# Performance work log

Hardware: AMD Instinct MI355X
Metric: run time of the kernel (lower is better)

The kernel has to match this reference:

```python
import jax, jax.numpy as jnp
import numpy as np

NC = 64
B, H, W = 32, 128, 128


def setup_inputs() -> dict:
    key = jax.random.key(0)
    kx, = jax.random.split(key, 1)
    x = jax.random.normal(kx, (B, NC, H, W), dtype=jnp.float32)
    # params as initialized in the torch module
    exp_param = jnp.eye(NC, dtype=jnp.float32)[:, :, None, None]  # (nc, nc, 1, 1)
    bias = jnp.zeros((NC, 1, 1), dtype=jnp.float32)               # (nc, 1, 1)
    return {"x": x, "exp_param": exp_param, "bias": bias}


def reference(x, exp_param, bias):
    # x: (B, nc, H, W); exp_param: (nc, nc, 1, 1); bias: (nc, 1, 1)
    xr = jax.nn.relu(x) + 0.1  # strictly positive -> log is safe
    # prod_i xr[b,i,h,w] ** E[i,j]  ==  exp( sum_i E[i,j] * log xr[b,i,h,w] )
    # Fused form avoids materializing the (B, nc, nc, H, W) intermediate.
    E = exp_param[:, :, 0, 0]  # (nc_in=i, nc_out=j)
    logx = jnp.log(xr)
    out = jnp.exp(jnp.einsum('bihw,ij->bjhw', logx, E)) + bias  # (B, nc, H, W)
    return out
```

## Files before the change

### kernel.cpp

```cpp
#include <hip/hip_runtime.h>

#define NCH 64
#define JT 32
#define NPASS (NCH / JT)
#define HWSZ 16384
#define NPOINTS (32 * HWSZ)

__global__ __launch_bounds__(256, 4) void fused_log_einsum_exp(
    const float* __restrict__ x,
    const float* __restrict__ E,
    const float* __restrict__ bias,
    float* __restrict__ out)
{
    const int p  = blockIdx.x * 256 + threadIdx.x;
    const int b  = p >> 14;
    const int hw = p & (HWSZ - 1);

    const float* xp = x   + (size_t)b * NCH * HWSZ + hw;
    float*       op = out + (size_t)b * NCH * HWSZ + hw;

    #pragma unroll 1
    for (int jt = 0; jt < NPASS; ++jt) {
        const float* Ej = E + jt * JT;

        float acc[JT];
        #pragma unroll
        for (int j = 0; j < JT; ++j) acc[j] = 0.0f;

        #pragma unroll 4
        for (int i = 0; i < NCH; ++i) {
            float v  = xp[(size_t)i * HWSZ];
            float lx = __logf(fmaxf(v, 0.0f) + 0.1f);
            #pragma unroll
            for (int j = 0; j < JT; ++j)
                acc[j] = fmaf(lx, Ej[i * NCH + j], acc[j]);
        }

        #pragma unroll
        for (int j = 0; j < JT; ++j)
            op[(size_t)(jt * JT + j) * HWSZ] = __expf(acc[j]) + bias[jt * JT + j];
    }
}

extern "C" void kernel_launch(void* const* d_in, const int* in_sizes, int n_in,
                              void* d_out, int out_size, void* d_ws, size_t ws_size,
                              hipStream_t stream) {
    const float* x    = (const float*)d_in[0];
    const float* E    = (const float*)d_in[1];
    const float* bias = (const float*)d_in[2];
    float* out = (float*)d_out;

    dim3 grid(NPOINTS / 256), block(256);
    hipLaunchKernelGGL(fused_log_einsum_exp, grid, block, 0, stream,
                       x, E, bias, out);
}
```

Before: 268.4 us.

## Cache all log values in registers and compute outputs row-wise via transposed E

Each thread now loads all 64 input channels once and keeps their logs in registers, instead of rereading x and recomputing the log in each of two output passes. The output loop now runs over j, so a small pre-kernel transposes E into workspace and each output row reads a contiguous E row. The dot product uses four partial accumulators. This halves global reads of x and the log work, but adds a second launch and raises register pressure against launch_bounds(256,4).

```diff
diff --git a/kernel.cpp b/kernel.cpp
--- a/kernel.cpp
+++ b/kernel.cpp
@@ -1,14 +1,24 @@
 #include <hip/hip_runtime.h>
 
 #define NCH 64
-#define JT 32
-#define NPASS (NCH / JT)
 #define HWSZ 16384
 #define NPOINTS (32 * HWSZ)
 
+__global__ __launch_bounds__(256) void transpose_E_kernel(
+    const float* __restrict__ E, float* __restrict__ ET)
+{
+    const int t = threadIdx.x;
+    #pragma unroll
+    for (int k = 0; k < 16; ++k) {
+        const int o = k * 256 + t;
+        const int j = o >> 6, i = o & 63;
+        ET[o] = E[i * NCH + j];
+    }
+}
+
 __global__ __launch_bounds__(256, 4) void fused_log_einsum_exp(
     const float* __restrict__ x,
-    const float* __restrict__ E,
+    const float* __restrict__ ET,
     const float* __restrict__ bias,
     float* __restrict__ out)
 {
@@ -19,26 +29,24 @@
     const float* xp = x   + (size_t)b * NCH * HWSZ + hw;
     float*       op = out + (size_t)b * NCH * HWSZ + hw;
 
+    float lx[NCH];
+    #pragma unroll
+    for (int i = 0; i < NCH; ++i) lx[i] = xp[(size_t)i * HWSZ];
+    #pragma unroll
+    for (int i = 0; i < NCH; ++i) lx[i] = __logf(fmaxf(lx[i], 0.0f) + 0.1f);
+
     #pragma unroll 1
-    for (int jt = 0; jt < NPASS; ++jt) {
-        const float* Ej = E + jt * JT;
-
-        float acc[JT];
+    for (int j = 0; j < NCH; ++j) {
+        const float* Er = ET + j * NCH;
+        float a0 = 0.f, a1 = 0.f, a2 = 0.f, a3 = 0.f;
         #pragma unroll
-        for (int j = 0; j < JT; ++j) acc[j] = 0.0f;
-
-        #pragma unroll 4
-        for (int i = 0; i < NCH; ++i) {
-            float v  = xp[(size_t)i * HWSZ];
-            float lx = __logf(fmaxf(v, 0.0f) + 0.1f);
-            #pragma unroll
-            for (int j = 0; j < JT; ++j)
-                acc[j] = fmaf(lx, Ej[i * NCH + j], acc[j]);
+        for (int i = 0; i < NCH; i += 4) {
+            a0 = fmaf(lx[i + 0], Er[i + 0], a0);
+            a1 = fmaf(lx[i + 1], Er[i + 1], a1);
+            a2 = fmaf(lx[i + 2], Er[i + 2], a2);
+            a3 = fmaf(lx[i + 3], Er[i + 3], a3);
         }
-
-        #pragma unroll
-        for (int j = 0; j < JT; ++j)
-            op[(size_t)(jt * JT + j) * HWSZ] = __expf(acc[j]) + bias[jt * JT + j];
+        op[(size_t)j * HWSZ] = __expf((a0 + a1) + (a2 + a3)) + bias[j];
     }
 }
 
@@ -49,8 +57,9 @@
     const float* E    = (const float*)d_in[1];
     const float* bias = (const float*)d_in[2];
     float* out = (float*)d_out;
+    float* ET  = (float*)d_ws;
 
-    dim3 grid(NPOINTS / 256), block(256);
-    hipLaunchKernelGGL(fused_log_einsum_exp, grid, block, 0, stream,
-                       x, E, bias, out);
+    hipLaunchKernelGGL(transpose_E_kernel, dim3(1), dim3(256), 0, stream, E, ET);
+    hipLaunchKernelGGL(fused_log_einsum_exp, dim3(NPOINTS / 256), dim3(256), 0,
+                       stream, x, ET, bias, out);
 }
```

After: 272.6 us. About the same (+1.6%).
